# Optimization experiments

Measured on AMD Instinct MI355X. Metric: run time of the kernel, lower is better.

## Reference

```python
import jax, jax.numpy as jnp
import numpy as np

C = 256
R = 16
K = 7

def setup_inputs() -> dict:
    key = jax.random.key(0)
    k1, k2, k3, k4 = jax.random.split(key, 4)
    x = jax.random.normal(k1, (16, C, 128, 128), dtype=jnp.float32)
    # PyTorch Linear weights: w1 [C//R, C], w2 [C, C//R]
    w1 = jax.random.normal(k2, (C // R, C), dtype=jnp.float32) * (1.0 / np.sqrt(C))
    w2 = jax.random.normal(k3, (C, C // R), dtype=jnp.float32) * (1.0 / np.sqrt(C // R))
    # Conv2d(2,1,K) weight: [out=1, in=2, K, K]
    wconv = jax.random.normal(k4, (1, 2, K, K), dtype=jnp.float32) * (1.0 / np.sqrt(2 * K * K))
    return {"x": x, "w1": w1, "w2": w2, "wconv": wconv}

def _mlp(v, w1, w2):  # v: [B, C]
    h = jax.nn.relu(v @ w1.T)  # [B, C//R]
    return h @ w2.T            # [B, C]

def reference(x, w1, w2, wconv):
    # channel attention
    avg = jnp.mean(x, axis=(2, 3))  # [B, C]
    mx = jnp.max(x, axis=(2, 3))    # [B, C]
    ch_att = jax.nn.sigmoid(_mlp(avg, w1, w2) + _mlp(mx, w1, w2))  # [B, C]
    x = x * ch_att[:, :, None, None]
    # spatial attention
    avg_sp = jnp.mean(x, axis=1, keepdims=True)  # [B,1,H,W]
    max_sp = jnp.max(x, axis=1, keepdims=True)   # [B,1,H,W]
    sp = jnp.concatenate([avg_sp, max_sp], axis=1)  # [B,2,H,W]
    conv = jax.lax.conv_general_dilated(
        sp, wconv, window_strides=(1, 1), padding=[(K // 2, K // 2)] * 2,
        dimension_numbers=("NCHW", "OIHW", "NCHW"))  # [B,1,H,W]
    sp_att = jax.nn.sigmoid(conv)
    return x * sp_att
```

## Files before the change

### kernel.cpp

```cpp
#include <hip/hip_runtime.h>
#include <hip/hip_fp16.h>
#include <math.h>

#define B   16
#define C   256
#define HW  16384
#define HW4 4096
#define HW8 2048
#define NCHUNK 8

typedef float vf4 __attribute__((ext_vector_type(4)));
typedef unsigned int vu4 __attribute__((ext_vector_type(4)));
typedef unsigned int vu2 __attribute__((ext_vector_type(2)));

__device__ __forceinline__ float2 h2f(unsigned int w) {
    __half2 h = *(const __half2*)&w;
    return __half22float2(h);
}

__device__ __forceinline__ float wave_reduce_sum(float v) {
    #pragma unroll
    for (int o = 32; o > 0; o >>= 1) v += __shfl_down(v, o, 64);
    return v;
}
__device__ __forceinline__ float wave_reduce_max(float v) {
    #pragma unroll
    for (int o = 32; o > 0; o >>= 1) v = fmaxf(v, __shfl_down(v, o, 64));
    return v;
}

__global__ __launch_bounds__(256) void k_chan_stats_cast(const float* __restrict__ x,
                                                         vu2* __restrict__ x16,
                                                         float* __restrict__ avg,
                                                         float* __restrict__ mx) {
    const int bc  = blockIdx.x;
    const int tid = threadIdx.x;
    const vf4* x4 = (const vf4*)x + (size_t)bc * HW4;
    vu2* o = x16 + (size_t)bc * HW4;
    float s = 0.f, m = -INFINITY;
    #pragma unroll
    for (int i = 0; i < 16; ++i) {
        vf4 v = __builtin_nontemporal_load(&x4[tid + i * 256]);
        s += (v.x + v.y) + (v.z + v.w);
        m = fmaxf(m, fmaxf(fmaxf(v.x, v.y), fmaxf(v.z, v.w)));
        __half2 lo = __halves2half2(__float2half_rn(v.x), __float2half_rn(v.y));
        __half2 hi = __halves2half2(__float2half_rn(v.z), __float2half_rn(v.w));
        vu2 u;
        u.x = *(const unsigned int*)&lo;
        u.y = *(const unsigned int*)&hi;
        o[tid + i * 256] = u;
    }
    s = wave_reduce_sum(s);
    m = wave_reduce_max(m);
    __shared__ float ss[4], sm[4];
    const int wid = tid >> 6, lane = tid & 63;
    if (lane == 0) { ss[wid] = s; sm[wid] = m; }
    __syncthreads();
    if (tid == 0) {
        float S = ss[0] + ss[1] + ss[2] + ss[3];
        float M = fmaxf(fmaxf(sm[0], sm[1]), fmaxf(sm[2], sm[3]));
        avg[bc] = S * (1.0f / HW);
        mx[bc]  = M;
    }
}

__global__ __launch_bounds__(256) void k_mlp(const float* __restrict__ avg,
                                             const float* __restrict__ mx,
                                             const float* __restrict__ w1,
                                             const float* __restrict__ w2,
                                             float* __restrict__ chatt) {
    const int b = blockIdx.x, tid = threadIdx.x;
    __shared__ float sa[C], sx[C], h[16];
    sa[tid] = avg[b * C + tid];
    sx[tid] = mx[b * C + tid];
    __syncthreads();
    if (tid < 16) {
        float ha = 0.f, hm = 0.f;
        for (int c2 = 0; c2 < C; ++c2) {
            float w = w1[tid * C + c2];
            ha += sa[c2] * w;
            hm += sx[c2] * w;
        }
        h[tid] = fmaxf(ha, 0.f) + fmaxf(hm, 0.f);
    }
    __syncthreads();
    float o = 0.f;
    #pragma unroll
    for (int j = 0; j < 16; ++j) o += h[j] * w2[tid * 16 + j];
    chatt[b * C + tid] = 1.0f / (1.0f + expf(-o));
}

__global__ __launch_bounds__(256) void k_sp_partial(const vu4* __restrict__ x16,
                                                    const float* __restrict__ chatt,
                                                    float* __restrict__ pavg,
                                                    float* __restrict__ pmax) {
    const int blk   = blockIdx.x;
    const int chunk = blk & 7;
    const int tile  = (blk >> 3) & 7;
    const int b     = blk >> 6;
    const int tid   = threadIdx.x;
    const int g     = tile * 256 + tid;
    float s[8];
    float m[8];
    #pragma unroll
    for (int k = 0; k < 8; ++k) { s[k] = 0.f; m[k] = -INFINITY; }
    const int c0 = chunk * 32;
    #pragma unroll 4
    for (int c = c0; c < c0 + 32; ++c) {
        vu4 u = x16[((size_t)(b * C + c)) * HW8 + g];
        const float a = chatt[b * C + c];
        #pragma unroll
        for (int q = 0; q < 4; ++q) {
            float2 f = h2f(u[q]);
            float y0 = f.x * a, y1 = f.y * a;
            s[2*q]   += y0;  s[2*q+1] += y1;
            m[2*q]   = fmaxf(m[2*q],   y0);
            m[2*q+1] = fmaxf(m[2*q+1], y1);
        }
    }
    vf4* pa = (vf4*)(pavg + ((size_t)(chunk * B + b)) * HW + g * 8);
    vf4* pm = (vf4*)(pmax + ((size_t)(chunk * B + b)) * HW + g * 8);
    vf4 a0 = {s[0], s[1], s[2], s[3]};
    vf4 a1 = {s[4], s[5], s[6], s[7]};
    vf4 m0 = {m[0], m[1], m[2], m[3]};
    vf4 m1 = {m[4], m[5], m[6], m[7]};
    pa[0] = a0; pa[1] = a1;
    pm[0] = m0; pm[1] = m1;
}

__global__ __launch_bounds__(256) void k_combine(const vf4* __restrict__ pavg,
                                                 const vf4* __restrict__ pmax,
                                                 vf4* __restrict__ cavg,
                                                 vf4* __restrict__ cmax) {
    const int i = blockIdx.x * 256 + threadIdx.x;
    vf4 s = {0.f, 0.f, 0.f, 0.f};
    vf4 m = {-INFINITY, -INFINITY, -INFINITY, -INFINITY};
    #pragma unroll
    for (int ch = 0; ch < NCHUNK; ++ch) {
        vf4 a = pavg[(size_t)ch * B * HW4 + i];
        vf4 x = pmax[(size_t)ch * B * HW4 + i];
        s += a;
        m.x = fmaxf(m.x, x.x); m.y = fmaxf(m.y, x.y);
        m.z = fmaxf(m.z, x.z); m.w = fmaxf(m.w, x.w);
    }
    s *= (1.0f / C);
    cavg[i] = s;
    cmax[i] = m;
}

__global__ __launch_bounds__(256) void k_conv(const float* __restrict__ cavg,
                                              const float* __restrict__ cmax,
                                              const float* __restrict__ wc,
                                              float* __restrict__ spatt) {
    const int idx = blockIdx.x * 256 + threadIdx.x;
    const int b = idx >> 14;
    const int p = idx & 16383;
    const int h = p >> 7, w = p & 127;
    __shared__ float swc[98];
    if (threadIdx.x < 98) swc[threadIdx.x] = wc[threadIdx.x];
    __syncthreads();
    const float* a  = cavg + b * HW;
    const float* mp = cmax + b * HW;
    float acc = 0.f;
    #pragma unroll
    for (int kh = 0; kh < 7; ++kh) {
        const int hi = h + kh - 3;
        if (hi < 0 || hi >= 128) continue;
        #pragma unroll
        for (int kw = 0; kw < 7; ++kw) {
            const int wi = w + kw - 3;
            if (wi < 0 || wi >= 128) continue;
            const int pi = hi * 128 + wi;
            acc += a[pi] * swc[kh * 7 + kw] + mp[pi] * swc[49 + kh * 7 + kw];
        }
    }
    spatt[idx] = 1.0f / (1.0f + expf(-acc));
}

__global__ __launch_bounds__(256) void k_final(const vu4* __restrict__ x16,
                                               const float* __restrict__ chatt,
                                               const vf4* __restrict__ spatt,
                                               vf4* __restrict__ out) {
    const size_t total  = (size_t)B * C * HW8;
    const size_t stride = (size_t)gridDim.x * 256;
    for (size_t f = (size_t)blockIdx.x * 256 + threadIdx.x; f < total; f += stride) {
        const size_t bc = f >> 11;
        const size_t g  = f & 2047;
        const size_t b  = bc >> 8;
        vu4 u = __builtin_nontemporal_load(&x16[f]);
        const float a = chatt[bc];
        vf4 sp0 = spatt[b * HW4 + g * 2];
        vf4 sp1 = spatt[b * HW4 + g * 2 + 1];
        float2 f0 = h2f(u.x);
        float2 f1 = h2f(u.y);
        float2 f2 = h2f(u.z);
        float2 f3 = h2f(u.w);
        vf4 r0, r1;
        r0.x = f0.x * a * sp0.x;  r0.y = f0.y * a * sp0.y;
        r0.z = f1.x * a * sp0.z;  r0.w = f1.y * a * sp0.w;
        r1.x = f2.x * a * sp1.x;  r1.y = f2.y * a * sp1.y;
        r1.z = f3.x * a * sp1.z;  r1.w = f3.y * a * sp1.w;
        __builtin_nontemporal_store(r0, &out[f * 2]);
        __builtin_nontemporal_store(r1, &out[f * 2 + 1]);
    }
}

extern "C" void kernel_launch(void* const* d_in, const int* in_sizes, int n_in,
                              void* d_out, int out_size, void* d_ws, size_t ws_size,
                              hipStream_t stream) {
    const float* x  = (const float*)d_in[0];
    const float* w1 = (const float*)d_in[1];
    const float* w2 = (const float*)d_in[2];
    const float* wc = (const float*)d_in[3];
    vf4* out = (vf4*)d_out;
    char* ws = (char*)d_ws;

    vu2* x16  = (vu2*)ws;
    char* p = ws + (size_t)B * C * HW * 2;
    float* avg   = (float*)p;            p += 4096 * 4;
    float* mx    = (float*)p;            p += 4096 * 4;
    float* chatt = (float*)p;            p += 4096 * 4;
    float* pavg  = (float*)p;            p += (size_t)NCHUNK * B * HW * 4;
    float* pmax  = (float*)p;            p += (size_t)NCHUNK * B * HW * 4;
    float* cavg  = (float*)p;            p += (size_t)B * HW * 4;
    float* cmax  = (float*)p;            p += (size_t)B * HW * 4;
    float* spatt = (float*)p;            p += (size_t)B * HW * 4;

    k_chan_stats_cast<<<B * C, 256, 0, stream>>>(x, x16, avg, mx);
    k_mlp<<<B, 256, 0, stream>>>(avg, mx, w1, w2, chatt);
    k_sp_partial<<<1024, 256, 0, stream>>>((const vu4*)x16, chatt, pavg, pmax);
    k_combine<<<256, 256, 0, stream>>>((const vf4*)pavg, (const vf4*)pmax,
                                       (vf4*)cavg, (vf4*)cmax);
    k_conv<<<B * HW / 256, 256, 0, stream>>>(cavg, cmax, wc, spatt);
    k_final<<<4096, 256, 0, stream>>>((const vu4*)x16, chatt,
                                      (const vf4*)spatt, (vf4*)out);
}
```

Baseline: 210.3 us.

## Fuse chunk combine into tiled shared-memory conv, halve channel chunks, parallelize MLP

Merges the partial-sum combine kernel into the 7x7 spatial conv. Each block now loads a 22x22 halo tile of reduced avg/max into shared memory and convolves from there, which removes the cavg/cmax round trip and one launch. The channel chunk count drops from 8 to 4, halving the partial buffers at the cost of fewer blocks (512) in the partial pass. The first MLP layer is spread across all 256 threads with shuffle reductions instead of 16 serial threads. The halo tile recomputes the combine at tile borders, so some work is duplicated.

```diff
diff --git a/kernel.cpp b/kernel.cpp
--- a/kernel.cpp
+++ b/kernel.cpp
@@ -7,7 +7,7 @@
 #define HW  16384
 #define HW4 4096
 #define HW8 2048
-#define NCHUNK 8
+#define NCHUNK 4
 
 typedef float vf4 __attribute__((ext_vector_type(4)));
 typedef unsigned int vu4 __attribute__((ext_vector_type(4)));
@@ -74,19 +74,24 @@
     sa[tid] = avg[b * C + tid];
     sx[tid] = mx[b * C + tid];
     __syncthreads();
-    if (tid < 16) {
-        float ha = 0.f, hm = 0.f;
-        for (int c2 = 0; c2 < C; ++c2) {
-            float w = w1[tid * C + c2];
-            ha += sa[c2] * w;
-            hm += sx[c2] * w;
-        }
-        h[tid] = fmaxf(ha, 0.f) + fmaxf(hm, 0.f);
-    }
+    const int j = tid >> 4, sub = tid & 15;
+    float pa = 0.f, pm = 0.f;
+    #pragma unroll
+    for (int c2 = sub; c2 < C; c2 += 16) {
+        float w = w1[j * C + c2];
+        pa += sa[c2] * w;
+        pm += sx[c2] * w;
+    }
+    #pragma unroll
+    for (int o = 8; o > 0; o >>= 1) {
+        pa += __shfl_down(pa, o, 16);
+        pm += __shfl_down(pm, o, 16);
+    }
+    if (sub == 0) h[j] = fmaxf(pa, 0.f) + fmaxf(pm, 0.f);
     __syncthreads();
     float o = 0.f;
     #pragma unroll
-    for (int j = 0; j < 16; ++j) o += h[j] * w2[tid * 16 + j];
+    for (int jj = 0; jj < 16; ++jj) o += h[jj] * w2[tid * 16 + jj];
     chatt[b * C + tid] = 1.0f / (1.0f + expf(-o));
 }
 
@@ -95,18 +100,18 @@
                                                     float* __restrict__ pavg,
                                                     float* __restrict__ pmax) {
     const int blk   = blockIdx.x;
-    const int chunk = blk & 7;
-    const int tile  = (blk >> 3) & 7;
-    const int b     = blk >> 6;
+    const int chunk = blk & 3;
+    const int tile  = (blk >> 2) & 7;
+    const int b     = blk >> 5;
     const int tid   = threadIdx.x;
     const int g     = tile * 256 + tid;
     float s[8];
     float m[8];
     #pragma unroll
     for (int k = 0; k < 8; ++k) { s[k] = 0.f; m[k] = -INFINITY; }
-    const int c0 = chunk * 32;
+    const int c0 = chunk * 64;
     #pragma unroll 4
-    for (int c = c0; c < c0 + 32; ++c) {
+    for (int c = c0; c < c0 + 64; ++c) {
         vu4 u = x16[((size_t)(b * C + c)) * HW8 + g];
         const float a = chatt[b * C + c];
         #pragma unroll
@@ -128,53 +133,46 @@
     pm[0] = m0; pm[1] = m1;
 }
 
-__global__ __launch_bounds__(256) void k_combine(const vf4* __restrict__ pavg,
-                                                 const vf4* __restrict__ pmax,
-                                                 vf4* __restrict__ cavg,
-                                                 vf4* __restrict__ cmax) {
-    const int i = blockIdx.x * 256 + threadIdx.x;
-    vf4 s = {0.f, 0.f, 0.f, 0.f};
-    vf4 m = {-INFINITY, -INFINITY, -INFINITY, -INFINITY};
-    #pragma unroll
-    for (int ch = 0; ch < NCHUNK; ++ch) {
-        vf4 a = pavg[(size_t)ch * B * HW4 + i];
-        vf4 x = pmax[(size_t)ch * B * HW4 + i];
-        s += a;
-        m.x = fmaxf(m.x, x.x); m.y = fmaxf(m.y, x.y);
-        m.z = fmaxf(m.z, x.z); m.w = fmaxf(m.w, x.w);
-    }
-    s *= (1.0f / C);
-    cavg[i] = s;
-    cmax[i] = m;
-}
-
-__global__ __launch_bounds__(256) void k_conv(const float* __restrict__ cavg,
-                                              const float* __restrict__ cmax,
-                                              const float* __restrict__ wc,
-                                              float* __restrict__ spatt) {
-    const int idx = blockIdx.x * 256 + threadIdx.x;
-    const int b = idx >> 14;
-    const int p = idx & 16383;
-    const int h = p >> 7, w = p & 127;
-    __shared__ float swc[98];
+__global__ __launch_bounds__(256) void k_comb_conv(const float* __restrict__ pavg,
+                                                   const float* __restrict__ pmax,
+                                                   const float* __restrict__ wc,
+                                                   float* __restrict__ spatt) {
+    const int blk = blockIdx.x;
+    const int tx = blk & 7, ty = (blk >> 3) & 7, b = blk >> 6;
+    __shared__ float sa[22][24], sm[22][24], swc[98];
     if (threadIdx.x < 98) swc[threadIdx.x] = wc[threadIdx.x];
-    __syncthreads();
-    const float* a  = cavg + b * HW;
-    const float* mp = cmax + b * HW;
+    for (int idx = threadIdx.x; idx < 484; idx += 256) {
+        const int ly = idx / 22, lx = idx - ly * 22;
+        const int gy = ty * 16 + ly - 3, gx = tx * 16 + lx - 3;
+        float s = 0.f, m = 0.f;
+        if (gy >= 0 && gy < 128 && gx >= 0 && gx < 128) {
+            const int p = gy * 128 + gx;
+            float mm = -INFINITY;
+            float ss = 0.f;
+            #pragma unroll
+            for (int ch = 0; ch < NCHUNK; ++ch) {
+                ss += pavg[(size_t)(ch * B + b) * HW + p];
+                mm = fmaxf(mm, pmax[(size_t)(ch * B + b) * HW + p]);
+            }
+            s = ss * (1.0f / C);
+            m = mm;
+        }
+        sa[ly][lx] = s;
+        sm[ly][lx] = m;
+    }
+    __syncthreads();
+    const int px = threadIdx.x & 15, py = threadIdx.x >> 4;
     float acc = 0.f;
     #pragma unroll
     for (int kh = 0; kh < 7; ++kh) {
-        const int hi = h + kh - 3;
-        if (hi < 0 || hi >= 128) continue;
         #pragma unroll
         for (int kw = 0; kw < 7; ++kw) {
-            const int wi = w + kw - 3;
-            if (wi < 0 || wi >= 128) continue;
-            const int pi = hi * 128 + wi;
-            acc += a[pi] * swc[kh * 7 + kw] + mp[pi] * swc[49 + kh * 7 + kw];
+            acc += sa[py + kh][px + kw] * swc[kh * 7 + kw]
+                 + sm[py + kh][px + kw] * swc[49 + kh * 7 + kw];
         }
     }
-    spatt[idx] = 1.0f / (1.0f + expf(-acc));
+    spatt[(size_t)b * HW + (ty * 16 + py) * 128 + tx * 16 + px] =
+        1.0f / (1.0f + expf(-acc));
 }
 
 __global__ __launch_bounds__(256) void k_final(const vu4* __restrict__ x16,
@@ -222,16 +220,12 @@
     float* chatt = (float*)p;            p += 4096 * 4;
     float* pavg  = (float*)p;            p += (size_t)NCHUNK * B * HW * 4;
     float* pmax  = (float*)p;            p += (size_t)NCHUNK * B * HW * 4;
-    float* cavg  = (float*)p;            p += (size_t)B * HW * 4;
-    float* cmax  = (float*)p;            p += (size_t)B * HW * 4;
     float* spatt = (float*)p;            p += (size_t)B * HW * 4;
 
     k_chan_stats_cast<<<B * C, 256, 0, stream>>>(x, x16, avg, mx);
     k_mlp<<<B, 256, 0, stream>>>(avg, mx, w1, w2, chatt);
-    k_sp_partial<<<1024, 256, 0, stream>>>((const vu4*)x16, chatt, pavg, pmax);
-    k_combine<<<256, 256, 0, stream>>>((const vf4*)pavg, (const vf4*)pmax,
-                                       (vf4*)cavg, (vf4*)cmax);
-    k_conv<<<B * HW / 256, 256, 0, stream>>>(cavg, cmax, wc, spatt);
+    k_sp_partial<<<512, 256, 0, stream>>>((const vu4*)x16, chatt, pavg, pmax);
+    k_comb_conv<<<1024, 256, 0, stream>>>(pavg, pmax, wc, spatt);
     k_final<<<4096, 256, 0, stream>>>((const vu4*)x16, chatt,
                                       (const vf4*)spatt, (vf4*)out);
 }
```

Measured after the change: 209.8 us. Within noise of the previous version (-0.2%).
